# Kernel tuning notes

Hardware: AMD Instinct MI355X
Metric: run time of the kernel (lower is better)

## Reference

```python
import jax, jax.numpy as jnp
import numpy as np

N, C, D, DOUT = 1024, 64, 16, 16   # nodes, channels, irreps_in dim (lmax=3), irreps_out dim
K3, K2, K1 = 16, 8, 4              # CG basis path counts per correlation order
NUM_ELEMENTS = 10


def _sym_basis(key, shape, sym_axes):
    """Random stand-in for e3nn reduced-CG U tensors: symmetrized over input axes."""
    u = jax.random.normal(key, shape, dtype=jnp.float32)
    acc = jnp.zeros(shape, jnp.float32)
    import itertools
    perms = list(itertools.permutations(sym_axes))
    for p in perms:
        order = list(range(len(shape)))
        for a, b in zip(sym_axes, p):
            order[a] = b
        acc = acc + jnp.transpose(u, order)
    return 0.05 * acc / len(perms)


def setup_inputs() -> dict:
    key = jax.random.key(0)
    ks = jax.random.split(key, 8)
    x = jax.random.normal(ks[0], (N, C, D), dtype=jnp.float32)
    indices = jax.random.randint(ks[1], (N,), 0, NUM_ELEMENTS, dtype=jnp.int32)
    w1 = jax.random.normal(ks[2], (NUM_ELEMENTS, K1, C), dtype=jnp.float32)
    w2 = jax.random.normal(ks[3], (NUM_ELEMENTS, K2, C), dtype=jnp.float32)
    w3 = jax.random.normal(ks[4], (NUM_ELEMENTS, K3, C), dtype=jnp.float32)
    U1 = _sym_basis(ks[5], (DOUT, D, K1), (1,))
    U2 = _sym_basis(ks[6], (DOUT, D, D, K2), (1, 2))
    U3 = _sym_basis(ks[7], (DOUT, D, D, D, K3), (1, 2, 3))
    return {"x": x, "indices": indices, "w1": w1, "w2": w2, "w3": w3,
            "U1": U1, "U2": U2, "U3": U3}


def reference(x, indices, w1, w2, w3, U1, U2, U3):
    # Per-node element selection of basis weights (replaces one-hot einsum 'ekc,be->bkc')
    w3s = w3[indices]  # [N, K3, C]
    w2s = w2[indices]  # [N, K2, C]
    w1s = w1[indices]  # [N, K1, C]

    # correlation 3: contract highest-order CG basis with weights and one copy of x
    # out[b,c,o,i,j] = sum_{l,k} U3[o,i,j,l,k] * w3s[b,k,c] * x[b,c,l]
    out = jnp.einsum('oijlk,bkc,bcl->bcoij', U3, w3s, x)

    # correlation 2: add weighted basis, contract one more copy of x
    out = out + jnp.einsum('oijk,bkc->bcoij', U2, w2s)
    out = jnp.einsum('bcoij,bcj->bcoi', out, x)

    # correlation 1: add weighted basis, contract last copy of x
    out = out + jnp.einsum('oik,bkc->bcoi', U1, w1s)
    out = jnp.einsum('bcoi,bci->bco', out, x)  # [N, C, DOUT]
    return out
```

## Files before the change

kernel.cpp:

```cpp
#include <hip/hip_runtime.h>
#include <hip/hip_bf16.h>

#define NCH 64
#define NEL 10
#define NSTEP 48

#define WS_OFFS   0
#define WS_LIST   1024
#define WS_W      2097152

typedef __attribute__((ext_vector_type(8))) short  short8v;
typedef __attribute__((ext_vector_type(4))) float  float4v;
typedef __attribute__((ext_vector_type(4))) int    int4v;

__host__ __device__ constexpr int PJF(int p) { int j = 0; while (p >= j + 1) { p -= j + 1; ++j; } return j; }
__host__ __device__ constexpr int PIF(int p) { int j = 0; while (p >= j + 1) { p -= j + 1; ++j; } return p; }
__host__ __device__ constexpr int PJH(int p) { int j = 8; while (p >= j + 1) { p -= j + 1; ++j; } return j; }
__host__ __device__ constexpr int PIH(int p) { int j = 8; while (p >= j + 1) { p -= j + 1; ++j; } return p; }

__device__ __forceinline__ unsigned int f_to_bf16u(float f) {
  union { float f; unsigned int i; } v; v.f = f;
  unsigned int x = v.i;
  unsigned int r = (x + 0x7fffu + ((x >> 16) & 1u)) >> 16;
  return r & 0xffffu;
}

__global__ __launch_bounds__(256) void k_bgemm(const float* __restrict__ U3,
                                               const float* __restrict__ U2,
                                               const float* __restrict__ U1,
                                               const float* __restrict__ w3,
                                               const float* __restrict__ w2,
                                               const float* __restrict__ w1,
                                               const int* __restrict__ idx,
                                               unsigned short* __restrict__ WK,
                                               int* __restrict__ ws_offs,
                                               int* __restrict__ ws_list) {
  __shared__ unsigned short sU[256 * 32];
  __shared__ unsigned short sWt[64 * 32];
  __shared__ char sLT[4][8192];
  __shared__ int cnt[NEL];
  __shared__ int base[NEL + 1];
  int b = blockIdx.x;
  int t = threadIdx.x;

  if (b == 960) {
    if (t < NEL) cnt[t] = 0;
    __syncthreads();
    int mye[4], myp[4];
#pragma unroll
    for (int k = 0; k < 4; ++k) {
      int n = t + k * 256;
      int e = idx[n];
      mye[k] = e;
      myp[k] = atomicAdd(&cnt[e], 1);
    }
    __syncthreads();
    if (t == 0) {
      int a = 0;
      for (int i = 0; i < NEL; ++i) { base[i] = a; a += cnt[i]; }
      base[NEL] = a;
    }
    __syncthreads();
#pragma unroll
    for (int k = 0; k < 4; ++k) ws_list[base[mye[k]] + myp[k]] = t + k * 256;
    if (t <= NEL) ws_offs[t] = base[t];
    return;
  }

  int e = b / 96, np = b - e * 96;
  int n0 = np * 2;

  {
    int o = t >> 4, dn = (t >> 3) & 1, jj = t & 7;
    int n = n0 + dn;
#pragma unroll
    for (int kq = 0; kq < 4; ++kq) {
      float v[8] = {0.f, 0.f, 0.f, 0.f, 0.f, 0.f, 0.f, 0.f};
      if (n < 172) {
        int ci, cj, h;
        if (n < 72) { int p = n >> 1; h = n & 1; int j = 0; while (p >= j + 1) { p -= j + 1; ++j; } ci = p; cj = j; }
        else        { int p = n - 72; h = 1;     int j = 8; while (p >= j + 1) { p -= j + 1; ++j; } ci = p; cj = j; }
        int l = h * 8 + jj;
        if (kq < 2 && l >= cj) {
          const float* line = U3 + ((((size_t)o * 16 + ci) * 16 + cj) * 16 + l) * 16 + kq * 8;
          float4 q0 = *(const float4*)line;
          float4 q1 = *(const float4*)(line + 4);
          float mult = (ci == cj) ? (cj == l ? 1.f : 3.f) : (cj == l ? 3.f : 6.f);
          v[0] = q0.x * mult; v[1] = q0.y * mult; v[2] = q0.z * mult; v[3] = q0.w * mult;
          v[4] = q1.x * mult; v[5] = q1.y * mult; v[6] = q1.z * mult; v[7] = q1.w * mult;
        }
      } else {
        int r = (n - 172) * 8 + jj;
        if (kq == 2 && r < 136) {
          int p = r, i2 = 0; while (p >= 16 - i2) { p -= 16 - i2; ++i2; }
          int a = i2, bb = i2 + p;
          const float* line = U2 + (((o * 16 + a) * 16) + bb) * 8;
          float4 q0 = *(const float4*)line;
          float4 q1 = *(const float4*)(line + 4);
          float sc = (a == bb) ? 1.f : 2.f;
          v[0] = q0.x * sc; v[1] = q0.y * sc; v[2] = q0.z * sc; v[3] = q0.w * sc;
          v[4] = q1.x * sc; v[5] = q1.y * sc; v[6] = q1.z * sc; v[7] = q1.w * sc;
        } else if (kq == 3 && r >= 136 && r < 152) {
          int a = r - 136;
          float4 q0 = *(const float4*)(U1 + (o * 16 + a) * 4);
          v[0] = q0.x; v[1] = q0.y; v[2] = q0.z; v[3] = q0.w;
        }
      }
      uint4 st;
      st.x = f_to_bf16u(v[0]) | (f_to_bf16u(v[1]) << 16);
      st.y = f_to_bf16u(v[2]) | (f_to_bf16u(v[3]) << 16);
      st.z = f_to_bf16u(v[4]) | (f_to_bf16u(v[5]) << 16);
      st.w = f_to_bf16u(v[6]) | (f_to_bf16u(v[7]) << 16);
      *(uint4*)(&sU[t * 32 + kq * 8]) = st;
    }
  }
  {
    int c = t & 63, kg = t >> 6;
    unsigned int pk[4];
#pragma unroll
    for (int hh = 0; hh < 4; ++hh) {
      int k0 = kg * 8 + hh * 2;
      float f0, f1;
      int k = k0;
      f0 = (k < 16) ? w3[(e * 16 + k) * NCH + c]
         : (k < 24) ? w2[(e * 8 + (k - 16)) * NCH + c]
         : (k < 28) ? w1[(e * 4 + (k - 24)) * NCH + c] : 0.f;
      k = k0 + 1;
      f1 = (k < 16) ? w3[(e * 16 + k) * NCH + c]
         : (k < 24) ? w2[(e * 8 + (k - 16)) * NCH + c]
         : (k < 28) ? w1[(e * 4 + (k - 24)) * NCH + c] : 0.f;
      pk[hh] = f_to_bf16u(f0) | (f_to_bf16u(f1) << 16);
    }
    uint4 st = {pk[0], pk[1], pk[2], pk[3]};
    *(uint4*)(&sWt[c * 32 + kg * 8]) = st;
  }
  __syncthreads();

  {
    int w = t >> 6, lane = t & 63;
    int rc2 = lane & 15, g2 = lane >> 4;
    int c = w * 16 + rc2;
    short8v bv = *(const short8v*)(sWt + c * 32 + g2 * 8);
    char* wb = &sLT[w][0];
    int wbyte = rc2 * 512 + (g2 >> 1) * 256 + (g2 & 1) * 8;

#pragma unroll 1
    for (int rt = 0; rt < 16; ++rt) {
      short8v av = *(const short8v*)(sU + (rt * 16 + rc2) * 32 + g2 * 8);
      float4v acc = {0.f, 0.f, 0.f, 0.f};
      acc = __builtin_amdgcn_mfma_f32_16x16x32_bf16(av, bv, acc, 0, 0, 0);
      unsigned int lo, hi;
      asm("v_cvt_pk_bf16_f32 %0, %1, %2" : "=v"(lo) : "v"(acc[0]), "v"(acc[1]));
      asm("v_cvt_pk_bf16_f32 %0, %1, %2" : "=v"(hi) : "v"(acc[2]), "v"(acc[3]));
      uint2 pk = {lo, hi};
      *(uint2*)(wb + wbyte + ((rt ^ rc2) & 15) * 16) = pk;
    }
    uint4* WK4 = (uint4*)WK;
    size_t ecw0 = (size_t)(e * 64 + w * 16);
    int KK0 = n0 >> 2, g0 = n0 & 3;
#pragma unroll
    for (int it = 0; it < 8; ++it) {
      int p = it * 64 + lane;
      int clocal = p >> 5, i5 = p & 31;
      int dn = i5 >> 4, o = i5 & 15;
      uint4 u = *(const uint4*)(wb + clocal * 512 + dn * 256 + ((o ^ clocal) & 15) * 16);
      size_t unit16 = ((ecw0 + clocal) * 48 + KK0) * 64 + (g0 + dn) * 16 + o;
      WK4[unit16] = u;
    }
  }
}

#define PACK_MFMA(M0, M1, M2, M3, M4, M5, M6, M7, KK, ACC) { \
  int b0, b1, b2, b3; \
  asm("v_cvt_pk_bf16_f32 %0, %1, %2" : "=v"(b0) : "v"(M0), "v"(M1)); \
  asm("v_cvt_pk_bf16_f32 %0, %1, %2" : "=v"(b1) : "v"(M2), "v"(M3)); \
  asm("v_cvt_pk_bf16_f32 %0, %1, %2" : "=v"(b2) : "v"(M4), "v"(M5)); \
  asm("v_cvt_pk_bf16_f32 %0, %1, %2" : "=v"(b3) : "v"(M6), "v"(M7)); \
  int4v ai = {b0, b1, b2, b3}; \
  short8v av = __builtin_bit_cast(short8v, ai); \
  short8v bv = *(const short8v*)(bkL + (KK) * 1024); \
  ACC = __builtin_amdgcn_mfma_f32_16x16x32_bf16(av, bv, ACC, 0, 0, 0); \
}

#define FULL_STEP(KK, ACC) { \
  constexpr int iA = PIF(2 * (KK)), jA = PJF(2 * (KK)); \
  constexpr int iB = PIF(2 * (KK) + 1), jB = PJF(2 * (KK) + 1); \
  float xxA = xr[iA] * xr[jA]; \
  float xxB = xr[iB] * xr[jB]; \
  float xx = selOdd ? xxB : xxA; \
  PACK_MFMA(xx * xsF[0], xx * xsF[1], xx * xsF[2], xx * xsF[3], \
            xx * xsF[4], xx * xsF[5], xx * xsF[6], xx * xsF[7], KK, ACC) \
}

#define H1_STEP(KK, ACC) { \
  constexpr int q = 4 * ((KK) - 18); \
  constexpr int i0 = PIH(q), j0 = PJH(q); \
  constexpr int i1 = PIH(q + 1), j1 = PJH(q + 1); \
  constexpr int i2 = PIH(q + 2), j2 = PJH(q + 2); \
  constexpr int i3 = PIH(q + 3), j3 = PJH(q + 3); \
  float xx0 = xr[i0] * xr[j0], xx1 = xr[i1] * xr[j1]; \
  float xx2 = xr[i2] * xr[j2], xx3 = xr[i3] * xr[j3]; \
  float xxE = selG1 ? xx1 : xx0; \
  float xxO = selG1 ? xx3 : xx2; \
  float xx = selOdd ? xxO : xxE; \
  PACK_MFMA(xx * xr[8], xx * xr[9], xx * xr[10], xx * xr[11], \
            xx * xr[12], xx * xr[13], xx * xr[14], xx * xr[15], KK, ACC) \
}

#define TAIL_STEP(KK, ACC) { \
  float mv[8]; \
  _Pragma("unroll") \
  for (int jj = 0; jj < 8; ++jj) { \
    int spec = sT[((KK) - 43) * 32 + g * 8 + jj]; \
    mv[jj] = sXw[spec & 31] * sXw[(spec >> 8) & 31]; \
  } \
  PACK_MFMA(mv[0], mv[1], mv[2], mv[3], mv[4], mv[5], mv[6], mv[7], KK, ACC) \
}

__global__ __launch_bounds__(512, 4) void k_main(const float* __restrict__ x,
                                                 const int* __restrict__ offs,
                                                 const int* __restrict__ list,
                                                 const unsigned short* __restrict__ WK,
                                                 float* __restrict__ out) {
  __shared__ unsigned short sB[NSTEP * 512];
  __shared__ float sX[8][16][18];
  __shared__ int sT[160];
  int t = threadIdx.x;
  int w = t >> 6, lane = t & 63;
  int rc = lane & 15;
  int g = lane >> 4;
  bool selOdd = g >= 2;
  bool selG1 = g & 1;

  int ec = blockIdx.x;
  int e = ec >> 6, c = ec & 63;

  int off = offs[e], nb = offs[e + 1] - off;
  int nt = (nb + 15) >> 4;
  const char* bkL = (const char*)sB + lane * 16;
  float* sXw = &sX[w][rc][0];

  int m0 = w * 16 + rc;
  int node0 = list[off + (m0 < nb ? m0 : (nb > 0 ? nb - 1 : 0))] & 1023;
  const float4* xp0 = (const float4*)(x + ((size_t)node0 * NCH + c) * 16);
  float4 p0 = xp0[0], p1 = xp0[1], p2 = xp0[2], p3 = xp0[3];

  {
    const uint4* Wg4 = (const uint4*)(WK + (size_t)ec * 24576);
    uint4* sB4 = (uint4*)sB;
#pragma unroll
    for (int s2 = 0; s2 < 6; ++s2) {
      __builtin_amdgcn_global_load_lds(
          (const __attribute__((address_space(1))) void*)(Wg4 + t + 512 * s2),
          (__attribute__((address_space(3))) void*)(sB4 + w * 64 + 512 * s2),
          16, 0, 0);
    }
  }
  if (t < 160) {
    int r = t, a, b2;
    if (r < 136) { int p = r, i2 = 0; while (p >= 16 - i2) { p -= 16 - i2; ++i2; } a = i2; b2 = i2 + p; }
    else if (r < 152) { a = r - 136; b2 = 16; }
    else { a = 17; b2 = 17; }
    sT[r] = a | (b2 << 8);
  }
  __syncthreads();

  for (int tile = w; tile < nt; tile += 8) {
    int node;
    float4 q0, q1, q2, q3;
    if (tile == w) {
      node = node0; q0 = p0; q1 = p1; q2 = p2; q3 = p3;
    } else {
      int m = tile * 16 + rc;
      node = list[off + (m < nb ? m : nb - 1)] & 1023;
      const float4* xp = (const float4*)(x + ((size_t)node * NCH + c) * 16);
      q0 = xp[0]; q1 = xp[1]; q2 = xp[2]; q3 = xp[3];
    }
    float xr[16];
    xr[0] = q0.x; xr[1] = q0.y; xr[2] = q0.z; xr[3] = q0.w;
    xr[4] = q1.x; xr[5] = q1.y; xr[6] = q1.z; xr[7] = q1.w;
    xr[8] = q2.x; xr[9] = q2.y; xr[10] = q2.z; xr[11] = q2.w;
    xr[12] = q3.x; xr[13] = q3.y; xr[14] = q3.z; xr[15] = q3.w;
    float xsF[8];
#pragma unroll
    for (int j = 0; j < 8; ++j) xsF[j] = selG1 ? xr[8 + j] : xr[j];
    if (g == 0) {
#pragma unroll
      for (int l = 0; l < 16; ++l) sXw[l] = xr[l];
      sXw[16] = 1.f; sXw[17] = 0.f;
    }

    float4v acc0 = {0.f, 0.f, 0.f, 0.f};
    float4v acc1 = {0.f, 0.f, 0.f, 0.f};
#define S2F(K) FULL_STEP(K, acc0) FULL_STEP((K) + 1, acc1)
#define S2H(K) H1_STEP(K, acc0) H1_STEP((K) + 1, acc1)
    S2F(0) S2F(2) S2F(4) S2F(6) S2F(8) S2F(10) S2F(12) S2F(14) S2F(16)
    S2H(18) S2H(20) S2H(22) S2H(24) S2H(26) S2H(28) S2H(30) S2H(32)
    S2H(34) S2H(36) S2H(38) S2H(40)
    H1_STEP(42, acc0)
    TAIL_STEP(43, acc1)
    TAIL_STEP(44, acc0) TAIL_STEP(45, acc1)
    TAIL_STEP(46, acc0) TAIL_STEP(47, acc1)
    float4v accs = acc0 + acc1;

#pragma unroll
    for (int r3 = 0; r3 < 4; ++r3) {
      int row = g * 4 + r3;
      int mrow = tile * 16 + row;
      if (mrow < nb) {
        int nd = __shfl(node, row);
        out[((size_t)nd * NCH + c) * 16 + rc] = accs[r3];
      }
    }
  }
}

extern "C" void kernel_launch(void* const* d_in, const int* in_sizes, int n_in,
                              void* d_out, int out_size, void* d_ws, size_t ws_size,
                              hipStream_t stream) {
  (void)in_sizes; (void)n_in; (void)out_size; (void)ws_size;
  const float* x   = (const float*)d_in[0];
  const int*   idx = (const int*)d_in[1];
  const float* w1  = (const float*)d_in[2];
  const float* w2  = (const float*)d_in[3];
  const float* w3  = (const float*)d_in[4];
  const float* U1  = (const float*)d_in[5];
  const float* U2  = (const float*)d_in[6];
  const float* U3  = (const float*)d_in[7];
  float* out = (float*)d_out;
  char* ws = (char*)d_ws;
  int* ws_offs = (int*)(ws + WS_OFFS);
  int* ws_list = (int*)(ws + WS_LIST);
  unsigned short* WK = (unsigned short*)(ws + WS_W);

  hipLaunchKernelGGL(k_bgemm, dim3(961), dim3(256), 0, stream, U3, U2, U1, w3, w2, w1,
                     idx, WK, ws_offs, ws_list);
  hipLaunchKernelGGL(k_main, dim3(640), dim3(512), 0, stream, x, ws_offs, ws_list, WK, out);
}
```

Before: 48.75 us.

## Double-buffer weight tiles in LDS in three chunks and store x as bf16

The full 48-step weight block is no longer loaded into shared memory up front. It is staged in three 16-step chunks through two 16 KB buffers, with each next chunk loaded asynchronously while the current chunk feeds the MFMAs. The per-wave x scratch is now stored as bf16, which shrinks LDS use further. The aim is to cut the LDS footprint so more blocks fit per CU. The cost is extra block-wide barriers in every batch and loop, redundant reloads of the weights for every batch, and lower precision in the tail products.

Result: slower. 50.19 us (+3.0%).

```diff
diff --git a/kernel.cpp b/kernel.cpp
--- a/kernel.cpp
+++ b/kernel.cpp
@@ -178,7 +178,7 @@
   asm("v_cvt_pk_bf16_f32 %0, %1, %2" : "=v"(b3) : "v"(M6), "v"(M7)); \
   int4v ai = {b0, b1, b2, b3}; \
   short8v av = __builtin_bit_cast(short8v, ai); \
-  short8v bv = *(const short8v*)(bkL + (KK) * 1024); \
+  short8v bv = *(const short8v*)(bkC + ((KK) & 15) * 1024); \
   ACC = __builtin_amdgcn_mfma_f32_16x16x32_bf16(av, bv, ACC, 0, 0, 0); \
 }
 
@@ -212,7 +212,10 @@
   _Pragma("unroll") \
   for (int jj = 0; jj < 8; ++jj) { \
     int spec = sT[((KK) - 43) * 32 + g * 8 + jj]; \
-    mv[jj] = sXw[spec & 31] * sXw[(spec >> 8) & 31]; \
+    union { unsigned u; float f; } fa, fb; \
+    fa.u = ((unsigned)sXw[spec & 31]) << 16; \
+    fb.u = ((unsigned)sXw[(spec >> 8) & 31]) << 16; \
+    mv[jj] = fa.f * fb.f; \
   } \
   PACK_MFMA(mv[0], mv[1], mv[2], mv[3], mv[4], mv[5], mv[6], mv[7], KK, ACC) \
 }
@@ -222,8 +225,8 @@
                                                  const int* __restrict__ list,
                                                  const unsigned short* __restrict__ WK,
                                                  float* __restrict__ out) {
-  __shared__ unsigned short sB[NSTEP * 512];
-  __shared__ float sX[8][16][18];
+  __shared__ unsigned short sB[2][8192];
+  __shared__ unsigned short sX[8][16][20];
   __shared__ int sT[160];
   int t = threadIdx.x;
   int w = t >> 6, lane = t & 63;
@@ -234,28 +237,27 @@
 
   int ec = blockIdx.x;
   int e = ec >> 6, c = ec & 63;
-
   int off = offs[e], nb = offs[e + 1] - off;
   int nt = (nb + 15) >> 4;
-  const char* bkL = (const char*)sB + lane * 16;
-  float* sXw = &sX[w][rc][0];
-
-  int m0 = w * 16 + rc;
-  int node0 = list[off + (m0 < nb ? m0 : (nb > 0 ? nb - 1 : 0))] & 1023;
-  const float4* xp0 = (const float4*)(x + ((size_t)node0 * NCH + c) * 16);
-  float4 p0 = xp0[0], p1 = xp0[1], p2 = xp0[2], p3 = xp0[3];
-
-  {
-    const uint4* Wg4 = (const uint4*)(WK + (size_t)ec * 24576);
-    uint4* sB4 = (uint4*)sB;
-#pragma unroll
-    for (int s2 = 0; s2 < 6; ++s2) {
-      __builtin_amdgcn_global_load_lds(
-          (const __attribute__((address_space(1))) void*)(Wg4 + t + 512 * s2),
-          (__attribute__((address_space(3))) void*)(sB4 + w * 64 + 512 * s2),
-          16, 0, 0);
-    }
-  }
+  int nbatch = (nt + 7) >> 3;
+  const uint4* Wg0 = (const uint4*)(WK + (size_t)ec * 24576);
+  uint4* sB4_0 = (uint4*)sB[0];
+  uint4* sB4_1 = (uint4*)sB[1];
+  const char* bk0 = (const char*)sB[0] + lane * 16;
+  const char* bk1 = (const char*)sB[1] + lane * 16;
+  unsigned short* sXw = &sX[w][rc][0];
+
+  auto STAGE = [&](int chunk3, uint4* dstbase) {
+    const uint4* src = Wg0 + chunk3 * 1024;
+    __builtin_amdgcn_global_load_lds(
+        (const __attribute__((address_space(1))) void*)(src + t),
+        (__attribute__((address_space(3))) void*)(dstbase + w * 64), 16, 0, 0);
+    __builtin_amdgcn_global_load_lds(
+        (const __attribute__((address_space(1))) void*)(src + 512 + t),
+        (__attribute__((address_space(3))) void*)(dstbase + 512 + w * 64), 16, 0, 0);
+  };
+
+  STAGE(0, sB4_0);
   if (t < 160) {
     int r = t, a, b2;
     if (r < 136) { int p = r, i2 = 0; while (p >= 16 - i2) { p -= 16 - i2; ++i2; } a = i2; b2 = i2 + p; }
@@ -263,14 +265,19 @@
     else { a = 17; b2 = 17; }
     sT[r] = a | (b2 << 8);
   }
+  int m0 = w * 16 + rc;
+  int node0 = list[off + (m0 < nb ? m0 : (nb > 0 ? nb - 1 : 0))] & 1023;
+  const float4* xp0 = (const float4*)(x + ((size_t)node0 * NCH + c) * 16);
+  float4 p0 = xp0[0], p1 = xp0[1], p2 = xp0[2], p3 = xp0[3];
   __syncthreads();
 
-  for (int tile = w; tile < nt; tile += 8) {
+  for (int batch = 0; batch < nbatch; ++batch) {
+    int bb = batch & 1;
+    int tile = w + 8 * batch;
     int node;
     float4 q0, q1, q2, q3;
-    if (tile == w) {
-      node = node0; q0 = p0; q1 = p1; q2 = p2; q3 = p3;
-    } else {
+    if (batch == 0) { node = node0; q0 = p0; q1 = p1; q2 = p2; q3 = p3; }
+    else {
       int m = tile * 16 + rc;
       node = list[off + (m < nb ? m : nb - 1)] & 1023;
       const float4* xp = (const float4*)(x + ((size_t)node * NCH + c) * 16);
@@ -286,17 +293,27 @@
     for (int j = 0; j < 8; ++j) xsF[j] = selG1 ? xr[8 + j] : xr[j];
     if (g == 0) {
 #pragma unroll
-      for (int l = 0; l < 16; ++l) sXw[l] = xr[l];
-      sXw[16] = 1.f; sXw[17] = 0.f;
+      for (int l = 0; l < 16; ++l) sXw[l] = (unsigned short)f_to_bf16u(xr[l]);
+      sXw[16] = 0x3F80; sXw[17] = 0;
     }
 
     float4v acc0 = {0.f, 0.f, 0.f, 0.f};
     float4v acc1 = {0.f, 0.f, 0.f, 0.f};
+    const char* bkC;
 #define S2F(K) FULL_STEP(K, acc0) FULL_STEP((K) + 1, acc1)
 #define S2H(K) H1_STEP(K, acc0) H1_STEP((K) + 1, acc1)
-    S2F(0) S2F(2) S2F(4) S2F(6) S2F(8) S2F(10) S2F(12) S2F(14) S2F(16)
-    S2H(18) S2H(20) S2H(22) S2H(24) S2H(26) S2H(28) S2H(30) S2H(32)
-    S2H(34) S2H(36) S2H(38) S2H(40)
+    STAGE(1, bb ? sB4_0 : sB4_1);
+    bkC = bb ? bk1 : bk0;
+    S2F(0) S2F(2) S2F(4) S2F(6) S2F(8) S2F(10) S2F(12) S2F(14)
+    __syncthreads();
+    STAGE(2, bb ? sB4_1 : sB4_0);
+    bkC = bb ? bk0 : bk1;
+    S2F(16)
+    S2H(18) S2H(20) S2H(22) S2H(24) S2H(26) S2H(28) S2H(30)
+    __syncthreads();
+    if (batch + 1 < nbatch) STAGE(0, bb ? sB4_0 : sB4_1);
+    bkC = bb ? bk1 : bk0;
+    S2H(32) S2H(34) S2H(36) S2H(38) S2H(40)
     H1_STEP(42, acc0)
     TAIL_STEP(43, acc1)
     TAIL_STEP(44, acc0) TAIL_STEP(45, acc1)
@@ -312,6 +329,7 @@
         out[((size_t)nd * NCH + c) * 16 + rc] = accs[r3];
       }
     }
+    __syncthreads();
   }
 }
 
```
